# Kernel optimization log

Hardware: AMD Instinct MI355X
Metric: run time of the kernel (lower is better)

The kernel has to match this reference:

```python
import jax, jax.numpy as jnp
import numpy as np

EPS = 1e-6

def layernorm(x, g, b):
    mu = jnp.mean(x, axis=-1, keepdims=True)
    var = jnp.mean(jnp.square(x - mu), axis=-1, keepdims=True)
    return (x - mu) * jax.lax.rsqrt(var + EPS) * g + b

def mlp(x, w1, b1, w2, b2):
    # torchvision MLPBlock: Linear -> GELU -> Linear (dropout=0)
    return jax.nn.gelu(x @ w1.T + b1, approximate=False) @ w2.T + b2

def mha(q, kv, w_in, b_in, w_out, b_out, h):
    # nn.MultiheadAttention (batch_first, self kv for key and value)
    B, Nq, E = q.shape
    Nk = kv.shape[1]
    hd = E // h
    wq, wk, wv = w_in[:E], w_in[E:2 * E], w_in[2 * E:]
    bq, bk, bv = b_in[:E], b_in[E:2 * E], b_in[2 * E:]
    Q = (q @ wq.T + bq).reshape(B, Nq, h, hd).transpose(0, 2, 1, 3)
    K = (kv @ wk.T + bk).reshape(B, Nk, h, hd).transpose(0, 2, 1, 3)
    V = (kv @ wv.T + bv).reshape(B, Nk, h, hd).transpose(0, 2, 1, 3)
    scores = jnp.einsum('bhqd,bhkd->bhqk', Q, K) / jnp.sqrt(jnp.float32(hd))
    attn = jax.nn.softmax(scores, axis=-1)
    out = jnp.einsum('bhqk,bhkd->bhqd', attn, V).transpose(0, 2, 1, 3).reshape(B, Nq, E)
    return out @ w_out.T + b_out

NUM_HEADS = 8

def _forward(inputs,
             ln_qf_g, ln_qf_b, ln_kvf_g, ln_kvf_b,
             ln_qb_g, ln_qb_b, ln_kvb_g, ln_kvb_b,
             fattn_w, fattn_b, fattn_ow, fattn_ob,
             battn_w, battn_b, battn_ow, battn_ob,
             mlpf_w1, mlpf_b1, mlpf_w2, mlpf_b2,
             mlpb_w1, mlpb_b1, mlpb_w2, mlpb_b2,
             resf_g, resf_b, resb_g, resb_b,
             ln2_g, ln2_b,
             mlp2_w1, mlp2_b1, mlp2_w2, mlp2_b2,
             lin_w, lin_b):
    b, n, nf, e = inputs.shape
    qf0 = inputs[:, 0]   # query_forward init
    qb0 = inputs[:, -1]  # query_backward init
    # per-step key/values: forward uses inputs[:, i], backward uses inputs[:, n-i-1], i = 1..n-1
    kvf_seq = jnp.swapaxes(inputs[:, 1:], 0, 1)                      # (n-1, B, Nf, E)
    kvb_seq = jnp.swapaxes(jnp.flip(inputs[:, :-1], axis=1), 0, 1)   # (n-1, B, Nf, E)

    def step(carry, xs):
        qf, qb = carry
        kvf, kvb = xs
        qf_ln = layernorm(qf, ln_qf_g, ln_qf_b)
        kvf_ln = layernorm(kvf, ln_kvf_g, ln_kvf_b)
        qb_ln = layernorm(qb, ln_qb_g, ln_qb_b)
        kvb_ln = layernorm(kvb, ln_kvb_g, ln_kvb_b)
        fav = mha(qf_ln, kvf_ln, fattn_w, fattn_b, fattn_ow, fattn_ob, NUM_HEADS)
        bav = mha(qb_ln, kvb_ln, battn_w, battn_b, battn_ow, battn_ob, NUM_HEADS)
        qf_new = layernorm(mlp(fav, mlpf_w1, mlpf_b1, mlpf_w2, mlpf_b2) + kvf_ln, resf_g, resf_b)
        qb_new = layernorm(mlp(bav, mlpb_w1, mlpb_b1, mlpb_w2, mlpb_b2) + kvb_ln, resb_g, resb_b)
        q = jnp.concatenate([qf_new, qb_new], axis=-1)  # (B, Nf, 2E)
        return (qf_new, qb_new), q

    _, qs = jax.lax.scan(step, (qf0, qb0), (kvf_seq, kvb_seq))
    attended = jnp.swapaxes(qs, 0, 1)  # (B, n-1, Nf, 2E)
    x = layernorm(attended, ln2_g, ln2_b)
    x = mlp(x, mlp2_w1, mlp2_b1, mlp2_w2, mlp2_b2)
    return x @ lin_w.T + lin_b  # (B, n-1, Nf, E)


def setup_inputs() -> dict:
    key = jax.random.key(0)
    ks = iter(jax.random.split(key, 64))
    def W(*shape):
        return (jax.random.normal(next(ks), shape, jnp.float32) * 0.02)
    B, N, NF, E, M = 32, 8, 256, 512, 2048
    d = {'inputs': jax.random.normal(next(ks), (B, N, NF, E), jnp.float32)}
    for nm in ['ln_qf', 'ln_kvf', 'ln_qb', 'ln_kvb', 'resf', 'resb']:
        d[nm + '_g'] = jnp.ones((E,), jnp.float32)
        d[nm + '_b'] = jnp.zeros((E,), jnp.float32)
    d['ln2_g'] = jnp.ones((2 * E,), jnp.float32)
    d['ln2_b'] = jnp.zeros((2 * E,), jnp.float32)
    for nm in ['fattn', 'battn']:
        d[nm + '_w'] = W(3 * E, E)
        d[nm + '_b'] = jnp.zeros((3 * E,), jnp.float32)
        d[nm + '_ow'] = W(E, E)
        d[nm + '_ob'] = jnp.zeros((E,), jnp.float32)
    for nm in ['mlpf', 'mlpb']:
        d[nm + '_w1'] = W(M, E)
        d[nm + '_b1'] = jnp.zeros((M,), jnp.float32)
        d[nm + '_w2'] = W(E, M)
        d[nm + '_b2'] = jnp.zeros((E,), jnp.float32)
    d['mlp2_w1'] = W(M, 2 * E)
    d['mlp2_b1'] = jnp.zeros((M,), jnp.float32)
    d['mlp2_w2'] = W(2 * E, M)
    d['mlp2_b2'] = jnp.zeros((2 * E,), jnp.float32)
    d['lin_w'] = W(E, 2 * E)
    d['lin_b'] = jnp.zeros((E,), jnp.float32)
    return d


def reference(inputs,
              ln_qf_g, ln_qf_b, ln_kvf_g, ln_kvf_b,
              ln_qb_g, ln_qb_b, ln_kvb_g, ln_kvb_b,
              fattn_w, fattn_b, fattn_ow, fattn_ob,
              battn_w, battn_b, battn_ow, battn_ob,
              mlpf_w1, mlpf_b1, mlpf_w2, mlpf_b2,
              mlpb_w1, mlpb_b1, mlpb_w2, mlpb_b2,
              resf_g, resf_b, resb_g, resb_b,
              ln2_g, ln2_b,
              mlp2_w1, mlp2_b1, mlp2_w2, mlp2_b2,
              lin_w, lin_b):
    return _forward(inputs,
                    ln_qf_g, ln_qf_b, ln_kvf_g, ln_kvf_b,
                    ln_qb_g, ln_qb_b, ln_kvb_g, ln_kvb_b,
                    fattn_w, fattn_b, fattn_ow, fattn_ob,
                    battn_w, battn_b, battn_ow, battn_ob,
                    mlpf_w1, mlpf_b1, mlpf_w2, mlpf_b2,
                    mlpb_w1, mlpb_b1, mlpb_w2, mlpb_b2,
                    resf_g, resf_b, resb_g, resb_b,
                    ln2_g, ln2_b,
                    mlp2_w1, mlp2_b1, mlp2_w2, mlp2_b2,
                    lin_w, lin_b)
```

## Files before the change

### kernel.cpp

```cpp
#include <hip/hip_runtime.h>
#include <hip/hip_bf16.h>

using bf16 = __hip_bfloat16;
typedef __attribute__((ext_vector_type(8))) __bf16 bf16x8;
typedef __attribute__((ext_vector_type(4))) float f32x4;

__device__ __forceinline__ float b2f(bf16 x) { return __bfloat162float(x); }
__device__ __forceinline__ bf16 f2b(float x) { return __float2bfloat16(x); }

__device__ __forceinline__ float gelu_fast(float x) {
    float y = fabsf(x) * 0.70710678118654752f;
    float t = 1.0f / (1.0f + 0.3275911f * y);
    float p = t * (0.254829592f + t * (-0.284496736f + t * (1.421413741f +
              t * (-1.453152027f + t * 1.061405429f))));
    float e = p * __expf(-y * y);
    float phi = (x >= 0.f) ? (1.0f - 0.5f * e) : (0.5f * e);
    return x * phi;
}

__device__ __forceinline__ void gl_lds16(const bf16* g, bf16* l) {
    __builtin_amdgcn_global_load_lds(
        (const __attribute__((address_space(1))) void*)g,
        (__attribute__((address_space(3))) void*)l,
        16, 0, 0);
}

__device__ __forceinline__ float blockSum256(float v, float* sc) {
    #pragma unroll
    for (int o = 32; o > 0; o >>= 1) v += __shfl_down(v, o, 64);
    __syncthreads();
    if ((threadIdx.x & 63) == 0) sc[threadIdx.x >> 6] = v;
    __syncthreads();
    return sc[0] + sc[1] + sc[2] + sc[3];
}

__global__ __launch_bounds__(256) void canon_kernel(
        const void* __restrict__ raw, const unsigned* __restrict__ probe,
        bf16* __restrict__ o16, float* __restrict__ o32, long n) {
    bool isf32 = (probe[0] == 0x3F800000u);
    long i = ((long)blockIdx.x * 256 + threadIdx.x) * 4;
    #pragma unroll
    for (int k = 0; k < 4; ++k) {
        long idx = i + k;
        if (idx < n) {
            float x = isf32 ? ((const float*)raw)[idx] : b2f(((const bf16*)raw)[idx]);
            if (o16) o16[idx] = f2b(x);
            if (o32) o32[idx] = x;
        }
    }
}

__global__ __launch_bounds__(256) void ln512_dual(
        const void* __restrict__ in, const unsigned* __restrict__ probe, int mode,
        long off0, long off1, long outerStride,
        const float* __restrict__ g0, const float* __restrict__ b0,
        const float* __restrict__ g1, const float* __restrict__ b1,
        float* __restrict__ out32, bf16* __restrict__ out16) {
    __shared__ float sc[4];
    int tid = threadIdx.x;
    long r = blockIdx.x;
    int ph = (int)(r >> 13);
    long rr = r & 8191;
    const float* g = ph ? g1 : g0;
    const float* bb = ph ? b1 : b0;
    long base = (ph ? off1 : off0) + (rr >> 8) * outerStride + (rr & 255) * 512;
    bool isbf = (mode == 1) || (mode == 2 && probe[0] != 0x3F800000u);
    float v0 = isbf ? b2f(((const bf16*)in)[base + tid])
                    : ((const float*)in)[base + tid];
    float v1 = isbf ? b2f(((const bf16*)in)[base + tid + 256])
                    : ((const float*)in)[base + tid + 256];
    float mu = blockSum256(v0 + v1, sc) * (1.f / 512.f);
    float d0 = v0 - mu, d1 = v1 - mu;
    float rs = rsqrtf(blockSum256(d0 * d0 + d1 * d1, sc) * (1.f / 512.f) + 1e-6f);
    float y0 = d0 * rs * g[tid] + bb[tid];
    float y1 = d1 * rs * g[tid + 256] + bb[tid + 256];
    long ro = r * 512;
    if (out32) { out32[ro + tid] = y0; out32[ro + tid + 256] = y1; }
    out16[ro + tid] = f2b(y0);
    out16[ro + tid + 256] = f2b(y1);
}

template<int E>
__global__ __launch_bounds__(256) void ln_rows(
        const void* __restrict__ in, const unsigned* __restrict__ probe, int mode,
        long baseOff, long outerStride,
        const float* __restrict__ g, const float* __restrict__ bb,
        float* __restrict__ out32, bf16* __restrict__ out16) {
    constexpr int NE = E / 256;
    __shared__ float sc[4];
    int tid = threadIdx.x;
    long r = blockIdx.x;
    bool isbf = (mode == 1) || (mode == 2 && probe[0] != 0x3F800000u);
    long off = baseOff + (r >> 8) * outerStride + (long)(r & 255) * E;
    float vv[NE];
    float s = 0.f;
    #pragma unroll
    for (int k = 0; k < NE; ++k) {
        long e = off + tid + (k << 8);
        float v = isbf ? b2f(((const bf16*)in)[e]) : ((const float*)in)[e];
        vv[k] = v; s += v;
    }
    float mu = blockSum256(s, sc) * (1.f / E);
    float vs = 0.f;
    #pragma unroll
    for (int k = 0; k < NE; ++k) { float d = vv[k] - mu; vs += d * d; }
    float rs = rsqrtf(blockSum256(vs, sc) * (1.f / E) + 1e-6f);
    long ro = r * (long)E;
    #pragma unroll
    for (int k = 0; k < NE; ++k) {
        int e = tid + (k << 8);
        float y = (vv[k] - mu) * rs * g[e] + bb[e];
        if (out32) out32[ro + e] = y;
        if (out16) out16[ro + e] = f2b(y);
    }
}

__global__ __launch_bounds__(256) void add_ln_dual(
        const float* __restrict__ a, const float* __restrict__ c,
        const float* __restrict__ g0, const float* __restrict__ b0,
        const float* __restrict__ g1, const float* __restrict__ b1,
        float* __restrict__ carry, bf16* __restrict__ att) {
    __shared__ float sc[4];
    int tid = threadIdx.x;
    long r = blockIdx.x;
    int ph = (int)(r >> 13);
    long rr = r & 8191;
    const float* g = ph ? g1 : g0;
    const float* bb = ph ? b1 : b0;
    float v0 = a[r * 512 + tid]       + c[r * 512 + tid];
    float v1 = a[r * 512 + tid + 256] + c[r * 512 + tid + 256];
    float mu = blockSum256(v0 + v1, sc) * (1.f / 512.f);
    float d0 = v0 - mu, d1 = v1 - mu;
    float rs = rsqrtf(blockSum256(d0 * d0 + d1 * d1, sc) * (1.f / 512.f) + 1e-6f);
    float y0 = d0 * rs * g[tid] + bb[tid];
    float y1 = d1 * rs * g[tid + 256] + bb[tid + 256];
    carry[r * 512 + tid] = y0;
    carry[r * 512 + tid + 256] = y1;
    att[rr * 1024 + ph * 512 + tid] = f2b(y0);
    att[rr * 1024 + ph * 512 + tid + 256] = f2b(y1);
}

template<int EPI>
__global__ __launch_bounds__(256) void gemm128d(
        const bf16* __restrict__ A,
        const bf16* __restrict__ W0, const bf16* __restrict__ W1,
        const float* __restrict__ bias0, const float* __restrict__ bias1,
        void* __restrict__ Cp, int M, int N, int K, int halfBm,
        int t, const unsigned* __restrict__ probe) {
    __shared__ bf16 As[128 * 32];
    __shared__ bf16 Bs[128 * 32];
    int tid = threadIdx.x;
    int lane = tid & 63, wave = tid >> 6;
    int bn = blockIdx.x, bm = blockIdx.y;
    int wr = wave >> 1, wc = wave & 1;
    const bf16* W = (bm >= halfBm) ? W1 : W0;
    const float* bias = (bm >= halfBm) ? bias1 : bias0;

    int srow = wave * 32 + (lane >> 2);
    int scol = (lane & 3) << 3;
    const bf16* aSrc = A + (long)(bm * 128 + srow) * K + scol;
    const bf16* wSrc = W + (long)(bn * 128 + srow) * K + scol;
    bf16* aDst = As + wave * 1024;
    bf16* bDst = Bs + wave * 1024;

    int r16 = lane & 15;
    int kq = lane >> 4;
    const bf16* aLds = As + (wr * 64 + r16) * 32 + kq * 8;
    const bf16* bLds = Bs + (wc * 64 + r16) * 32 + kq * 8;

    f32x4 acc[4][4] = {};
    for (int k0 = 0; k0 < K; k0 += 32) {
        gl_lds16(aSrc + k0,             aDst);
        gl_lds16(aSrc + k0 + 16L * K,   aDst + 512);
        gl_lds16(wSrc + k0,             bDst);
        gl_lds16(wSrc + k0 + 16L * K,   bDst + 512);
        __syncthreads();
        bf16x8 af[4], bg[4];
        #pragma unroll
        for (int m = 0; m < 4; ++m) af[m] = *(const bf16x8*)(aLds + m * 16 * 32);
        #pragma unroll
        for (int n = 0; n < 4; ++n) bg[n] = *(const bf16x8*)(bLds + n * 16 * 32);
        #pragma unroll
        for (int m = 0; m < 4; ++m)
            #pragma unroll
            for (int n = 0; n < 4; ++n)
                acc[m][n] = __builtin_amdgcn_mfma_f32_16x16x32_bf16(
                    af[m], bg[n], acc[m][n], 0, 0, 0);
        __syncthreads();
    }

    int row0 = bm * 128 + wr * 64 + kq * 4;
    int col0 = bn * 128 + wc * 64 + r16;
    #pragma unroll
    for (int n = 0; n < 4; ++n) {
        int col = col0 + n * 16;
        float bv = bias[col];
        #pragma unroll
        for (int m = 0; m < 4; ++m) {
            #pragma unroll
            for (int i = 0; i < 4; ++i) {
                float v = acc[m][n][i] + bv;
                long row = row0 + m * 16 + i;
                if (EPI == 2) v = gelu_fast(v);
                if (EPI == 0) {
                    ((float*)Cp)[row * (long)N + col] = v;
                } else if (EPI == 3) {
                    long b = row >> 8, f = row & 255;
                    long off = b * 917504 + (long)t * 131072 + f * 512 + col;
                    if (probe[0] == 0x3F800000u) ((float*)Cp)[off] = v;
                    else                         ((bf16*)Cp)[off] = f2b(v);
                } else {
                    ((bf16*)Cp)[row * (long)N + col] = f2b(v);
                }
            }
        }
    }
}

__global__ __launch_bounds__(256) void attn_mfma(
        const bf16* __restrict__ Q, const bf16* __restrict__ KV,
        bf16* __restrict__ O) {
    __shared__ bf16 Vt[64 * 264];
    __shared__ float S[32 * 260];
    bf16* P = (bf16*)S;
    int tid = threadIdx.x;
    int lane = tid & 63, wave = tid >> 6;
    int r16 = lane & 15, kq = lane >> 4;
    int yy = blockIdx.y;
    int ph = yy >> 8, b = (yy & 255) >> 3, h = yy & 7;
    int hf = blockIdx.x;
    long rowbase = (long)ph * 8192 + (long)b * 256;

    {
        const bf16* vsrc = KV + (rowbase + tid) * 1024 + 512 + h * 64;
        bf16 vrow[64];
        #pragma unroll
        for (int c = 0; c < 8; ++c)
            *(bf16x8*)(vrow + c * 8) = *(const bf16x8*)(vsrc + c * 8);
        #pragma unroll
        for (int d = 0; d < 64; ++d)
            Vt[d * 264 + tid] = vrow[d];
    }
    __syncthreads();

    const bf16* Qb = Q + (rowbase + hf * 128) * 512 + h * 64;
    const bf16* Kb = KV + rowbase * 1024 + h * 64;

    for (int qt = 0; qt < 4; ++qt) {
        int q0 = qt * 32;
        f32x4 sacc[2][4] = {};
        #pragma unroll
        for (int k0 = 0; k0 < 64; k0 += 32) {
            bf16x8 aq[2], bk[4];
            #pragma unroll
            for (int m = 0; m < 2; ++m)
                aq[m] = *(const bf16x8*)(Qb + (long)(q0 + m * 16 + r16) * 512 + k0 + kq * 8);
            #pragma unroll
            for (int n = 0; n < 4; ++n)
                bk[n] = *(const bf16x8*)(Kb + (long)(wave * 64 + n * 16 + r16) * 1024 + k0 + kq * 8);
            #pragma unroll
            for (int m = 0; m < 2; ++m)
                #pragma unroll
                for (int n = 0; n < 4; ++n)
                    sacc[m][n] = __builtin_amdgcn_mfma_f32_16x16x32_bf16(
                        aq[m], bk[n], sacc[m][n], 0, 0, 0);
        }
        #pragma unroll
        for (int m = 0; m < 2; ++m)
            #pragma unroll
            for (int n = 0; n < 4; ++n)
                #pragma unroll
                for (int i = 0; i < 4; ++i)
                    S[(m * 16 + kq * 4 + i) * 260 + wave * 64 + n * 16 + r16] =
                        sacc[m][n][i] * 0.125f;
        __syncthreads();
        int row = tid >> 3, cl = tid & 7;
        float pv[32];
        float mx = -1e30f;
        #pragma unroll
        for (int j = 0; j < 32; ++j) {
            pv[j] = S[row * 260 + cl + 8 * j];
            mx = fmaxf(mx, pv[j]);
        }
        mx = fmaxf(mx, __shfl_xor(mx, 1, 64));
        mx = fmaxf(mx, __shfl_xor(mx, 2, 64));
        mx = fmaxf(mx, __shfl_xor(mx, 4, 64));
        float sm = 0.f;
        #pragma unroll
        for (int j = 0; j < 32; ++j) { pv[j] = __expf(pv[j] - mx); sm += pv[j]; }
        sm += __shfl_xor(sm, 1, 64);
        sm += __shfl_xor(sm, 2, 64);
        sm += __shfl_xor(sm, 4, 64);
        float inv = 1.f / sm;
        __syncthreads();
        #pragma unroll
        for (int j = 0; j < 32; ++j)
            P[row * 264 + cl + 8 * j] = f2b(pv[j] * inv);
        __syncthreads();
        f32x4 oacc[2] = {{0.f,0.f,0.f,0.f},{0.f,0.f,0.f,0.f}};
        #pragma unroll
        for (int ks = 0; ks < 8; ++ks) {
            bf16x8 ap0 = *(const bf16x8*)(P + (r16) * 264 + ks * 32 + kq * 8);
            bf16x8 ap1 = *(const bf16x8*)(P + (16 + r16) * 264 + ks * 32 + kq * 8);
            bf16x8 bv  = *(const bf16x8*)(Vt + (wave * 16 + r16) * 264 + ks * 32 + kq * 8);
            oacc[0] = __builtin_amdgcn_mfma_f32_16x16x32_bf16(ap0, bv, oacc[0], 0, 0, 0);
            oacc[1] = __builtin_amdgcn_mfma_f32_16x16x32_bf16(ap1, bv, oacc[1], 0, 0, 0);
        }
        bf16* Ob = O + (rowbase + hf * 128 + q0) * 512 + h * 64 + wave * 16 + r16;
        #pragma unroll
        for (int m = 0; m < 2; ++m)
            #pragma unroll
            for (int i = 0; i < 4; ++i)
                Ob[(long)(m * 16 + kq * 4 + i) * 512] = f2b(oacc[m][i]);
        __syncthreads();
    }
}

extern "C" void kernel_launch(void* const* d_in, const int* in_sizes, int n_in,
                              void* d_out, int out_size, void* d_ws, size_t ws_size,
                              hipStream_t stream) {
    (void)in_sizes; (void)n_in; (void)out_size; (void)ws_size;
    const unsigned* probe = (const unsigned*)d_in[1];

    char* base = (char*)d_ws;
    size_t off = 0;
    auto alloc = [&](size_t bytes) -> void* {
        void* p = base + off;
        off = (off + bytes + 255) & ~(size_t)255;
        return p;
    };

    bf16* fw  = (bf16*)alloc(786432 * 2);
    bf16* bw  = (bf16*)alloc(786432 * 2);
    bf16* fow = (bf16*)alloc(262144 * 2);
    bf16* bow = (bf16*)alloc(262144 * 2);
    bf16* fw1 = (bf16*)alloc(1048576 * 2);
    bf16* fw2 = (bf16*)alloc(1048576 * 2);
    bf16* bw1 = (bf16*)alloc(1048576 * 2);
    bf16* bw2 = (bf16*)alloc(1048576 * 2);
    bf16* w21 = (bf16*)alloc(2097152 * 2);
    bf16* w22 = (bf16*)alloc(2097152 * 2);
    bf16* lw  = (bf16*)alloc(524288 * 2);

    float* f32c[40] = {};
    const int  sIdx[] = {1,2,3,4,5,6,7,8,9,10,11,12,13,14,16,18,20,22,24,26,28,30,32,34,36};
    const long sN[]   = {512,512,512,512,512,512,512,512,512,512,512,512,1024,1024,
                         1536,512,1536,512,2048,512,2048,512,2048,1024,512};
    for (int k = 0; k < 25; ++k) f32c[sIdx[k]] = (float*)alloc(sN[k] * 4);

    float* carry   = (float*)alloc(8388608 * 4);
    bf16*  lnq16   = (bf16*) alloc(8388608 * 2);
    bf16*  lnkv16  = (bf16*) alloc(8388608 * 2);
    float* lnkv32  = (float*)alloc(8388608 * 4);
    void*  u_qm    = alloc(8388608 * 4);
    bf16*  Qbuf    = (bf16*)u_qm;
    float* mlpo32  = (float*)u_qm;
    bf16*  KVbuf   = (bf16*) alloc(16777216 * 2);
    bf16*  att16   = (bf16*) alloc(8388608 * 2);
    bf16*  fav16   = (bf16*) alloc(8388608 * 2);
    bf16*  hid16   = (bf16*) alloc(33554432 * 2);
    bf16*  attended= (bf16*) alloc(58720256 * 2);
    bf16*  xln16   = att16;
    bf16*  h2      = hid16;
    bf16*  x2      = fav16;

    auto canon = [&](int idx, long n, bf16* o16, float* o32) {
        int grid = (int)((n + 1023) >> 10);
        canon_kernel<<<grid, 256, 0, stream>>>(d_in[idx], probe, o16, o32, n);
    };
    canon(15, 786432, fw,  nullptr);
    canon(19, 786432, bw,  nullptr);
    canon(17, 262144, fow, nullptr);
    canon(21, 262144, bow, nullptr);
    canon(23, 1048576, fw1, nullptr);
    canon(25, 1048576, fw2, nullptr);
    canon(27, 1048576, bw1, nullptr);
    canon(29, 1048576, bw2, nullptr);
    canon(31, 2097152, w21, nullptr);
    canon(33, 2097152, w22, nullptr);
    canon(35, 524288, lw, nullptr);
    for (int k = 0; k < 25; ++k) canon(sIdx[k], sN[k], nullptr, f32c[sIdx[k]]);

    const long SLICE = 131072;
    const long BSTRIDE = 1048576;

    for (int t = 0; t < 7; ++t) {
        if (t == 0)
            ln512_dual<<<16384, 256, 0, stream>>>(d_in[0], probe, 2,
                0 * SLICE, 7 * SLICE, BSTRIDE,
                f32c[1], f32c[2], f32c[5], f32c[6], nullptr, lnq16);
        else
            ln512_dual<<<16384, 256, 0, stream>>>(carry, probe, 0,
                0, 4194304, 131072,
                f32c[1], f32c[2], f32c[5], f32c[6], nullptr, lnq16);
        ln512_dual<<<16384, 256, 0, stream>>>(d_in[0], probe, 2,
            (t + 1) * SLICE, (long)(6 - t) * SLICE, BSTRIDE,
            f32c[3], f32c[4], f32c[7], f32c[8], lnkv32, lnkv16);
        gemm128d<1><<<dim3(4, 128), 256, 0, stream>>>(lnq16, fw, bw,
            f32c[16], f32c[20], Qbuf, 16384, 512, 512, 64, 0, nullptr);
        gemm128d<1><<<dim3(8, 128), 256, 0, stream>>>(lnkv16,
            fw + 512 * 512, bw + 512 * 512, f32c[16] + 512, f32c[20] + 512,
            KVbuf, 16384, 1024, 512, 64, 0, nullptr);
        attn_mfma<<<dim3(2, 512), 256, 0, stream>>>(Qbuf, KVbuf, att16);
        gemm128d<1><<<dim3(4, 128), 256, 0, stream>>>(att16, fow, bow,
            f32c[18], f32c[22], fav16, 16384, 512, 512, 64, 0, nullptr);
        gemm128d<2><<<dim3(16, 128), 256, 0, stream>>>(fav16, fw1, bw1,
            f32c[24], f32c[28], hid16, 16384, 2048, 512, 64, 0, nullptr);
        gemm128d<0><<<dim3(4, 128), 256, 0, stream>>>(hid16, fw2, bw2,
            f32c[26], f32c[30], mlpo32, 16384, 512, 2048, 64, 0, nullptr);
        add_ln_dual<<<16384, 256, 0, stream>>>(mlpo32, lnkv32,
            f32c[9], f32c[10], f32c[11], f32c[12],
            carry, attended + (long)t * 8388608);
    }

    for (int t = 0; t < 7; ++t) {
        ln_rows<1024><<<8192, 256, 0, stream>>>(attended + (long)t * 8388608,
            probe, 1, 0, 262144, f32c[13], f32c[14], nullptr, xln16);
        gemm128d<2><<<dim3(16, 64), 256, 0, stream>>>(xln16, w21, w21,
            f32c[32], f32c[32], h2, 8192, 2048, 1024, 64, 0, nullptr);
        gemm128d<1><<<dim3(8, 64), 256, 0, stream>>>(h2, w22, w22,
            f32c[34], f32c[34], x2, 8192, 1024, 2048, 64, 0, nullptr);
        gemm128d<3><<<dim3(4, 64), 256, 0, stream>>>(x2, lw, lw,
            f32c[36], f32c[36], d_out, 8192, 512, 1024, 64, t, probe);
    }
}
```

Baseline: 3.830 ms.

## Double-buffer GEMM LDS tiles with BK=64 to overlap loads and MFMA

```diff
diff --git a/kernel.cpp b/kernel.cpp
--- a/kernel.cpp
+++ b/kernel.cpp
@@ -141,52 +141,71 @@
 }
 
 template<int EPI>
-__global__ __launch_bounds__(256) void gemm128d(
+__global__ __launch_bounds__(256) void gemm2ph(
         const bf16* __restrict__ A,
         const bf16* __restrict__ W0, const bf16* __restrict__ W1,
         const float* __restrict__ bias0, const float* __restrict__ bias1,
         void* __restrict__ Cp, int M, int N, int K, int halfBm,
         int t, const unsigned* __restrict__ probe) {
-    __shared__ bf16 As[128 * 32];
-    __shared__ bf16 Bs[128 * 32];
+    __shared__ bf16 As[2][8192];
+    __shared__ bf16 Bs[2][8192];
     int tid = threadIdx.x;
-    int lane = tid & 63, wave = tid >> 6;
+    int lane = tid & 63, wid = tid >> 6;
     int bn = blockIdx.x, bm = blockIdx.y;
-    int wr = wave >> 1, wc = wave & 1;
+    int wr = wid >> 1, wc = wid & 1;
     const bf16* W = (bm >= halfBm) ? W1 : W0;
     const float* bias = (bm >= halfBm) ? bias1 : bias0;
 
-    int srow = wave * 32 + (lane >> 2);
-    int scol = (lane & 3) << 3;
-    const bf16* aSrc = A + (long)(bm * 128 + srow) * K + scol;
-    const bf16* wSrc = W + (long)(bn * 128 + srow) * K + scol;
-    bf16* aDst = As + wave * 1024;
-    bf16* bDst = Bs + wave * 1024;
+    int srow0 = wid * 32 + (lane >> 3);
+    int scol  = (lane & 7) << 3;
+    const bf16* aS = A + (long)(bm * 128 + srow0) * K + scol;
+    const bf16* wS = W + (long)(bn * 128 + srow0) * K + scol;
+    int dbase = wid * 2048;
 
     int r16 = lane & 15;
     int kq = lane >> 4;
-    const bf16* aLds = As + (wr * 64 + r16) * 32 + kq * 8;
-    const bf16* bLds = Bs + (wc * 64 + r16) * 32 + kq * 8;
 
     f32x4 acc[4][4] = {};
-    for (int k0 = 0; k0 < K; k0 += 32) {
-        gl_lds16(aSrc + k0,             aDst);
-        gl_lds16(aSrc + k0 + 16L * K,   aDst + 512);
-        gl_lds16(wSrc + k0,             bDst);
-        gl_lds16(wSrc + k0 + 16L * K,   bDst + 512);
+    int nt = K >> 6;
+
+    #pragma unroll
+    for (int j = 0; j < 4; ++j) {
+        gl_lds16(aS + (long)(j * 8) * K, &As[0][dbase + j * 512]);
+        gl_lds16(wS + (long)(j * 8) * K, &Bs[0][dbase + j * 512]);
+    }
+    __syncthreads();
+
+    int cur = 0;
+    for (int kt = 0; kt < nt; ++kt) {
+        if (kt + 1 < nt) {
+            long ko = (long)(kt + 1) << 6;
+            #pragma unroll
+            for (int j = 0; j < 4; ++j) {
+                gl_lds16(aS + (long)(j * 8) * K + ko, &As[cur ^ 1][dbase + j * 512]);
+                gl_lds16(wS + (long)(j * 8) * K + ko, &Bs[cur ^ 1][dbase + j * 512]);
+            }
+        }
+        bf16x8 af[2][4], bg[2][4];
+        #pragma unroll
+        for (int kh = 0; kh < 2; ++kh) {
+            #pragma unroll
+            for (int m = 0; m < 4; ++m)
+                af[kh][m] = *(const bf16x8*)(&As[cur][(wr * 64 + m * 16 + r16) * 64 + kh * 32 + kq * 8]);
+            #pragma unroll
+            for (int n = 0; n < 4; ++n)
+                bg[kh][n] = *(const bf16x8*)(&Bs[cur][(wc * 64 + n * 16 + r16) * 64 + kh * 32 + kq * 8]);
+        }
+        #pragma unroll
+        for (int m = 0; m < 4; ++m)
+            #pragma unroll
+            for (int n = 0; n < 4; ++n) {
+                acc[m][n] = __builtin_amdgcn_mfma_f32_16x16x32_bf16(
+                    af[0][m], bg[0][n], acc[m][n], 0, 0, 0);
+                acc[m][n] = __builtin_amdgcn_mfma_f32_16x16x32_bf16(
+                    af[1][m], bg[1][n], acc[m][n], 0, 0, 0);
+            }
         __syncthreads();
-        bf16x8 af[4], bg[4];
-        #pragma unroll
-        for (int m = 0; m < 4; ++m) af[m] = *(const bf16x8*)(aLds + m * 16 * 32);
-        #pragma unroll
-        for (int n = 0; n < 4; ++n) bg[n] = *(const bf16x8*)(bLds + n * 16 * 32);
-        #pragma unroll
-        for (int m = 0; m < 4; ++m)
-            #pragma unroll
-            for (int n = 0; n < 4; ++n)
-                acc[m][n] = __builtin_amdgcn_mfma_f32_16x16x32_bf16(
-                    af[m], bg[n], acc[m][n], 0, 0, 0);
-        __syncthreads();
+        cur ^= 1;
     }
 
     int row0 = bm * 128 + wr * 64 + kq * 4;
@@ -396,17 +415,17 @@
         ln512_dual<<<16384, 256, 0, stream>>>(d_in[0], probe, 2,
             (t + 1) * SLICE, (long)(6 - t) * SLICE, BSTRIDE,
             f32c[3], f32c[4], f32c[7], f32c[8], lnkv32, lnkv16);
-        gemm128d<1><<<dim3(4, 128), 256, 0, stream>>>(lnq16, fw, bw,
+        gemm2ph<1><<<dim3(4, 128), 256, 0, stream>>>(lnq16, fw, bw,
             f32c[16], f32c[20], Qbuf, 16384, 512, 512, 64, 0, nullptr);
-        gemm128d<1><<<dim3(8, 128), 256, 0, stream>>>(lnkv16,
+        gemm2ph<1><<<dim3(8, 128), 256, 0, stream>>>(lnkv16,
             fw + 512 * 512, bw + 512 * 512, f32c[16] + 512, f32c[20] + 512,
             KVbuf, 16384, 1024, 512, 64, 0, nullptr);
         attn_mfma<<<dim3(2, 512), 256, 0, stream>>>(Qbuf, KVbuf, att16);
-        gemm128d<1><<<dim3(4, 128), 256, 0, stream>>>(att16, fow, bow,
+        gemm2ph<1><<<dim3(4, 128), 256, 0, stream>>>(att16, fow, bow,
             f32c[18], f32c[22], fav16, 16384, 512, 512, 64, 0, nullptr);
-        gemm128d<2><<<dim3(16, 128), 256, 0, stream>>>(fav16, fw1, bw1,
+        gemm2ph<2><<<dim3(16, 128), 256, 0, stream>>>(fav16, fw1, bw1,
             f32c[24], f32c[28], hid16, 16384, 2048, 512, 64, 0, nullptr);
-        gemm128d<0><<<dim3(4, 128), 256, 0, stream>>>(hid16, fw2, bw2,
+        gemm2ph<0><<<dim3(4, 128), 256, 0, stream>>>(hid16, fw2, bw2,
             f32c[26], f32c[30], mlpo32, 16384, 512, 2048, 64, 0, nullptr);
         add_ln_dual<<<16384, 256, 0, stream>>>(mlpo32, lnkv32,
             f32c[9], f32c[10], f32c[11], f32c[12],
@@ -416,11 +435,11 @@
     for (int t = 0; t < 7; ++t) {
         ln_rows<1024><<<8192, 256, 0, stream>>>(attended + (long)t * 8388608,
             probe, 1, 0, 262144, f32c[13], f32c[14], nullptr, xln16);
-        gemm128d<2><<<dim3(16, 64), 256, 0, stream>>>(xln16, w21, w21,
+        gemm2ph<2><<<dim3(16, 64), 256, 0, stream>>>(xln16, w21, w21,
             f32c[32], f32c[32], h2, 8192, 2048, 1024, 64, 0, nullptr);
-        gemm128d<1><<<dim3(8, 64), 256, 0, stream>>>(h2, w22, w22,
+        gemm2ph<1><<<dim3(8, 64), 256, 0, stream>>>(h2, w22, w22,
             f32c[34], f32c[34], x2, 8192, 1024, 2048, 64, 0, nullptr);
-        gemm128d<3><<<dim3(4, 64), 256, 0, stream>>>(x2, lw, lw,
+        gemm2ph<3><<<dim3(4, 64), 256, 0, stream>>>(x2, lw, lw,
             f32c[36], f32c[36], d_out, 8192, 512, 1024, 64, t, probe);
     }
 }
```

After: 3.627 ms. -5.3%, faster.
